# Kernel tuning notes

Hardware: AMD Instinct MI355X
Metric: run time of the kernel (lower is better)

Reference implementation:

```python
import jax, jax.numpy as jnp
import numpy as np

DT = 0.01
Ek, El, Ena = -77.0, -65.0, 55.0
Iapp, Kp, Vt, Vs = 1.5, 3.0, 20.0, 0.0
a_d, a_r = 1.0, 0.1
gk, gl, gna, gs = 35.0, 0.3, 40.0, 0.04
B, T = 100, 2000


def _safe(num, den, fallback):
    # Reproduces the torch.where singularity patch at V==25 / V==-35.
    z = den == 0
    return jnp.where(z, fallback, num / jnp.where(z, 1.0, den))


def _rates(V):
    aN = _safe(0.02 * (V - 25), 1 - jnp.exp((25 - V) / 9.0), 0.18)
    bN = _safe(-0.002 * (V - 25), 1 - jnp.exp((V - 25) / 9.0), 0.018)
    aM = _safe(0.182 * (V + 35), 1 - jnp.exp((-V - 35) / 9.0), 1.638)
    bM = _safe(-0.124 * (V + 35), 1 - jnp.exp((V + 35) / 9.0), 1.116)
    aH = 0.25 * jnp.exp((-V - 90) / 12.0)
    bH = 0.25 * jnp.exp((V + 34) / 12.0)
    return aN, bN, aM, bM, aH, bH


def _gate(a, b, prev):
    # Crank-Nicolson gate update: (a*DT + (1 - DT/2*(a+b))*prev) / (DT/2*(a+b) + 1)
    s = DT / 2 * (a + b)
    return (a * DT + (1 - s) * prev) / (s + 1)


def _hh_layer(z, y0):
    # z: (B, T, N) synaptic drive; returns full voltage history (B, T, N).
    Bn, Tn, N = z.shape
    V0 = jnp.full((Bn, N), -70.0, z.dtype)
    init = (V0, jnp.zeros_like(V0), jnp.zeros_like(V0),
            jnp.ones_like(V0), jnp.full_like(V0, y0))
    zp = jnp.transpose(z[:, :-1, :], (1, 0, 2))  # z[k-1] drives step k

    def step(c, zk):
        V, m, n, h, y = c
        p1 = gna * m ** 3 * h
        p2 = gk * n ** 4
        Gs = DT / 2 * (p1 + p2 + gl + gs * y)
        E = p1 * Ena + p2 * Ek + gl * El + gs * Vs * y
        Vn = (V * (1 - Gs) + DT * (E + Iapp)) / (1 + Gs)
        aN, bN, aM, bM, aH, bH = _rates(Vn)
        mn = _gate(aM, bM, m)
        nn = _gate(aN, bN, n)
        hn = _gate(aH, bH, h)
        yn = _gate(a_d * zk, a_r, y)
        return (Vn, mn, nn, hn, yn), Vn

    _, Vh = jax.lax.scan(step, init, zp)  # (T-1, B, N)
    return jnp.concatenate([V0[None], Vh], 0).transpose(1, 0, 2)


def setup_inputs() -> dict:
    key = jax.random.key(0)
    k1, k2, k3 = jax.random.split(key, 3)
    batch = jax.random.normal(k1, (B, T, 28 * 28), jnp.float32)
    W1 = jax.random.normal(k2, (100, 28 * 28), jnp.float32) / np.sqrt(28 * 28)
    W2 = jax.random.normal(k3, (10, 100), jnp.float32) / np.sqrt(100)
    return {"batch": batch, "W1": W1, "W2": W2}


def reference(batch, W1, W2):
    z1 = jnp.einsum('bti,oi->bto', batch, W1)          # (B,T,100)
    V1 = _hh_layer(z1, 0.0)
    T1 = jax.nn.sigmoid((V1 - Vt) / Kp)
    z2 = jnp.einsum('btn,on->bto', T1, W2)             # (B,T,10)
    V2 = _hh_layer(z2, 1.0)
    return jax.nn.sigmoid((V2 - Vt) / Kp)
```

## Files before the change

### kernel.cpp

```cpp
#include <hip/hip_runtime.h>

#define TT 2000
#define NB 100
#define N1 100
#define KIN 784
#define CT1 1998
#define NC1 10000
#define CT2 1999
#define NC2 1000
#define NPAD 112
#define KPAD 800
#define S1 128
#define NCHUNK 16

typedef __attribute__((ext_vector_type(8))) short bf16x8;
typedef __attribute__((ext_vector_type(4))) float f32x4;

__device__ __forceinline__ float rcp_f(float d) { return __builtin_amdgcn_rcpf(d); }
__device__ __forceinline__ float sigmoid3(float V) {
  return rcp_f(1.0f + __expf((20.0f - V) * (1.0f / 3.0f)));
}
__device__ __forceinline__ float sig_from_u(float u) {
  float u3 = u * u * u;
  return rcp_f(1.0f + 0.18887560f * u3);
}
__device__ __forceinline__ float gate_u(float a, float b, float p) {
  float s = 0.005f * (a + b);
  return (a * 0.01f + (1.0f - s) * p) * rcp_f(s + 1.0f);
}
__device__ __forceinline__ float hh_step(float& V, float& m, float& n, float& h,
                                         float& y, float ay, float by, float ry) {
  float p1 = 40.0f * m * m * m * h;
  float nn2 = n * n;
  float p2 = 35.0f * nn2 * nn2;
  float Gs = 0.005f * (p1 + p2 + 0.3f + 0.04f * y);
  float E = p1 * 55.0f + p2 * (-77.0f) + (0.3f * (-65.0f));
  float Vn = (V * (1.0f - Gs) + 0.01f * (E + 1.5f)) * rcp_f(1.0f + Gs);

  float u_n = __expf((25.0f - Vn) * (1.0f / 9.0f));
  float u_m = __expf((-Vn - 35.0f) * (1.0f / 9.0f));
  float aH  = 0.25f * __expf((-Vn - 90.0f) * (1.0f / 12.0f));
  float bH  = 0.25f * __expf((Vn + 34.0f) * (1.0f / 12.0f));

  float dn = 1.0f - u_n, dm = 1.0f - u_m;
  float Bn = 0.02f * (Vn - 25.0f);
  float Am = 0.182f * (Vn + 35.0f);
  if (dn == 0.0f) { Bn = 0.18f;  dn = 1.0f; }
  if (dm == 0.0f) { Am = 1.638f; dm = 1.0f; }
  float Pn = 0.005f * Bn * (1.0f + 0.1f * u_n);
  float Pm = 0.005f * Am * (1.0f + 0.6813187f * u_m);
  n = (Bn * 0.01f + (dn - Pn) * n) * rcp_f(dn + Pn);
  m = (Am * 0.01f + (dm - Pm) * m) * rcp_f(dm + Pm);
  h = gate_u(aH, bH, h);
  y = (ay + by * y) * ry;
  V = Vn;
  return u_n;
}

__device__ __forceinline__ short bf16rne(float x) {
  unsigned u = __builtin_bit_cast(unsigned, x);
  unsigned r = u + 0x7fffu + ((u >> 16) & 1u);
  return (short)(r >> 16);
}
__device__ __forceinline__ float bf2f(short s) {
  unsigned u = ((unsigned)(unsigned short)s) << 16;
  return __builtin_bit_cast(float, u);
}
__device__ __forceinline__ void bsplit(float x, short& h, short& l) {
  h = bf16rne(x);
  l = bf16rne(x - bf2f(h));
}

__global__ __launch_bounds__(256) void prep_w1(const float* __restrict__ W1,
                                               short* __restrict__ W1h,
                                               short* __restrict__ W1l) {
  int idx = blockIdx.x * 256 + threadIdx.x;
  if (idx >= NPAD * KPAD) return;
  int nrow = idx / KPAD, k = idx - nrow * KPAD;
  float v = (nrow < N1 && k < KIN) ? W1[nrow * KIN + k] : 0.0f;
  short h, l; bsplit(v, h, l);
  W1h[idx] = h; W1l[idx] = l;
}

__device__ void gemm_body(const float* __restrict__ batch, const short* __restrict__ W1h,
                          const short* __restrict__ W1l, float* __restrict__ z1s,
                          int k, int b, char* smem) {
  short (*AsH)[32] = (short(*)[32])(smem);
  short (*AsL)[32] = (short(*)[32])(smem + 8192);
  short (*BsH)[32] = (short(*)[32])(smem + 16384);
  short (*BsL)[32] = (short(*)[32])(smem + 16384 + 7168);

  const int tid = threadIdx.x;
  const int tBeg = k * S1;
  const int tEnd = (tBeg + S1 < CT1) ? (tBeg + S1) : CT1;
  const int rows = tEnd - tBeg;
  const size_t rBeg = (size_t)b * CT1 + tBeg;

  const int w = tid >> 6;
  const int lane = tid & 63;
  const int lr = lane & 15;
  const int kg = lane >> 4;
  const int srow = tid >> 1;
  const int kc = (tid & 1) * 16;
  const int brow = tid >> 1;
  const bool bAct = (tid < 224);

  int tCl = tBeg + ((srow < rows) ? srow : (rows - 1));
  const float* aSrc = batch + ((size_t)b * TT + tCl) * KIN + kc;
  const short* bhSrc = W1h + (size_t)brow * KPAD + kc;
  const short* blSrc = W1l + (size_t)brow * KPAD + kc;

  float4 a0, a1, a2, a3;
  int4 bh0, bh1, bl0, bl1;

  a0 = a1 = a2 = a3 = make_float4(0.f, 0.f, 0.f, 0.f);
  if (kc < KIN) {
    a0 = *(const float4*)(aSrc);
    a1 = *(const float4*)(aSrc + 4);
    a2 = *(const float4*)(aSrc + 8);
    a3 = *(const float4*)(aSrc + 12);
  }
  if (bAct) {
    bh0 = *(const int4*)(bhSrc);
    bh1 = *(const int4*)(bhSrc + 8);
    bl0 = *(const int4*)(blSrc);
    bl1 = *(const int4*)(blSrc + 8);
  }

  f32x4 acc[2][7];
#pragma unroll
  for (int mt = 0; mt < 2; ++mt)
#pragma unroll
    for (int nt = 0; nt < 7; ++nt) acc[mt][nt] = (f32x4){0.f, 0.f, 0.f, 0.f};

  for (int kt = 0; kt < KPAD; kt += 32) {
    __syncthreads();
    {
      float av[16] = {a0.x, a0.y, a0.z, a0.w, a1.x, a1.y, a1.z, a1.w,
                      a2.x, a2.y, a2.z, a2.w, a3.x, a3.y, a3.z, a3.w};
      bf16x8 h0, h1, l0, l1;
#pragma unroll
      for (int i = 0; i < 8; ++i) {
        short hh, ll;
        bsplit(av[i], hh, ll);     h0[i] = hh; l0[i] = ll;
        bsplit(av[8 + i], hh, ll); h1[i] = hh; l1[i] = ll;
      }
      *(bf16x8*)&AsH[srow][kc] = h0;
      *(bf16x8*)&AsH[srow][kc + 8] = h1;
      *(bf16x8*)&AsL[srow][kc] = l0;
      *(bf16x8*)&AsL[srow][kc + 8] = l1;
      if (bAct) {
        *(int4*)&BsH[brow][kc] = bh0;
        *(int4*)&BsH[brow][kc + 8] = bh1;
        *(int4*)&BsL[brow][kc] = bl0;
        *(int4*)&BsL[brow][kc + 8] = bl1;
      }
    }
    __syncthreads();

    int kn = kt + 32;
    if (kn < KPAD) {
      a0 = a1 = a2 = a3 = make_float4(0.f, 0.f, 0.f, 0.f);
      if (kn + kc < KIN) {
        a0 = *(const float4*)(aSrc + kn);
        a1 = *(const float4*)(aSrc + kn + 4);
        a2 = *(const float4*)(aSrc + kn + 8);
        a3 = *(const float4*)(aSrc + kn + 12);
      }
      if (bAct) {
        bh0 = *(const int4*)(bhSrc + kn);
        bh1 = *(const int4*)(bhSrc + kn + 8);
        bl0 = *(const int4*)(blSrc + kn);
        bl1 = *(const int4*)(blSrc + kn + 8);
      }
    }

    bf16x8 aH0 = *(bf16x8*)&AsH[w * 32 + lr][kg * 8];
    bf16x8 aH1 = *(bf16x8*)&AsH[w * 32 + 16 + lr][kg * 8];
    bf16x8 aL0 = *(bf16x8*)&AsL[w * 32 + lr][kg * 8];
    bf16x8 aL1 = *(bf16x8*)&AsL[w * 32 + 16 + lr][kg * 8];
#pragma unroll
    for (int nt = 0; nt < 7; ++nt) {
      bf16x8 bH = *(bf16x8*)&BsH[nt * 16 + lr][kg * 8];
      bf16x8 bL = *(bf16x8*)&BsL[nt * 16 + lr][kg * 8];
      acc[0][nt] = __builtin_amdgcn_mfma_f32_16x16x32_bf16(aH0, bH, acc[0][nt], 0, 0, 0);
      acc[0][nt] = __builtin_amdgcn_mfma_f32_16x16x32_bf16(aH0, bL, acc[0][nt], 0, 0, 0);
      acc[0][nt] = __builtin_amdgcn_mfma_f32_16x16x32_bf16(aL0, bH, acc[0][nt], 0, 0, 0);
      acc[1][nt] = __builtin_amdgcn_mfma_f32_16x16x32_bf16(aH1, bH, acc[1][nt], 0, 0, 0);
      acc[1][nt] = __builtin_amdgcn_mfma_f32_16x16x32_bf16(aH1, bL, acc[1][nt], 0, 0, 0);
      acc[1][nt] = __builtin_amdgcn_mfma_f32_16x16x32_bf16(aL1, bH, acc[1][nt], 0, 0, 0);
    }
  }

#pragma unroll
  for (int nt = 0; nt < 7; ++nt) {
    int n = nt * 16 + lr;
    if (n < 100) {
#pragma unroll
      for (int mt = 0; mt < 2; ++mt) {
        int rloc = w * 32 + mt * 16 + kg * 4;
        f32x4 d = acc[mt][nt];
#pragma unroll
        for (int rr = 0; rr < 4; ++rr) {
          if (rloc + rr < rows) z1s[(rBeg + rloc + rr) * 100 + n] = d[rr];
        }
      }
    }
  }
}

__device__ void l1_body(const float* __restrict__ z1s, float* __restrict__ T1s,
                        float* __restrict__ st, int k, int lb) {
  int c = lb * 256 + threadIdx.x;
  if (c >= NC1) return;
  int b = c / 100, ni = c - b * 100;
  int tBeg = k * S1;
  int tEnd = (tBeg + S1 < CT1) ? (tBeg + S1) : CT1;
  int nsteps = tEnd - tBeg;
  float* SV = st; float* SM = st + NC1; float* SN = st + 2 * NC1;
  float* SH = st + 3 * NC1; float* SY = st + 4 * NC1;
  float V, m, n, h, y;
  if (k == 0) {
    V = -70.f; m = 0.f; n = 0.f; h = 1.f; y = 0.f;
    T1s[c] = __expf((25.0f + 70.0f) * (1.0f / 9.0f));
  } else { V = SV[c]; m = SM[c]; n = SN[c]; h = SH[c]; y = SY[c]; }
  const float* zp = z1s + ((size_t)b * CT1 + tBeg) * 100 + ni;
  float* tp = T1s + (size_t)(tBeg + 1) * NC1 + c;
  float zc[8], zx[8], ay[8], by[8], ry[8];
#pragma unroll
  for (int j = 0; j < 8; ++j) zc[j] = zp[j * 100];
  zp += 800;
  int NW = nsteps >> 3, tail = nsteps & 7;
  for (int i = 0; i < NW; ++i) {
#pragma unroll
    for (int j = 0; j < 8; ++j) zx[j] = zp[j * 100];
    zp += 800;
#pragma unroll
    for (int j = 0; j < 8; ++j) {
      float s = 0.005f * zc[j] + 0.0005f;
      ay[j] = zc[j] * 0.01f; by[j] = 1.0f - s; ry[j] = rcp_f(1.0f + s);
    }
#pragma unroll
    for (int j = 0; j < 8; ++j) {
      float u = hh_step(V, m, n, h, y, ay[j], by[j], ry[j]);
      *tp = u;
      tp += NC1;
    }
#pragma unroll
    for (int j = 0; j < 8; ++j) zc[j] = zx[j];
  }
  for (int j = 0; j < tail; ++j) {
    float s = 0.005f * zc[j] + 0.0005f;
    float u = hh_step(V, m, n, h, y, zc[j] * 0.01f, 1.0f - s, rcp_f(1.0f + s));
    *tp = u;
    tp += NC1;
  }
  SV[c] = V; SM[c] = m; SN[c] = n; SH[c] = h; SY[c] = y;
}

__device__ void z2_body(const float* __restrict__ T1s, const float* __restrict__ W2,
                        float* __restrict__ z2s, int k, int zb, char* smem) {
  float* w2 = (float*)smem;
  const int tid = threadIdx.x;
  if (tid < 250) *(float4*)&w2[tid * 4] = *(const float4*)&W2[tid * 4];
  __syncthreads();
  int tBeg = k * S1;
  int tEnd = (tBeg + S1 < CT2) ? (tBeg + S1) : CT2;
  int r = tBeg * NB + zb * 256 + tid;
  if (r >= tEnd * NB) return;
  const float* in = T1s + (size_t)r * 100;
  float acc[10];
#pragma unroll
  for (int o = 0; o < 10; ++o) acc[o] = 0.f;
  for (int k4 = 0; k4 < 25; ++k4) {
    float4 v = *(const float4*)(in + k4 * 4);
    v.x = sig_from_u(v.x); v.y = sig_from_u(v.y);
    v.z = sig_from_u(v.z); v.w = sig_from_u(v.w);
#pragma unroll
    for (int o = 0; o < 10; ++o) {
      float4 w = *(const float4*)&w2[o * 100 + k4 * 4];
      acc[o] += v.x * w.x + v.y * w.y + v.z * w.z + v.w * w.w;
    }
  }
  float* op = z2s + (size_t)r * 10;
#pragma unroll
  for (int o = 0; o < 10; o += 2) *(float2*)(op + o) = make_float2(acc[o], acc[o + 1]);
}

__device__ void l2_body(const float* __restrict__ z2s, float* __restrict__ out,
                        float* __restrict__ st, int k, int lb) {
  int c2 = lb * 256 + threadIdx.x;
  if (c2 >= NC2) return;
  int b = c2 / 10, o = c2 - b * 10;
  int tBeg = k * S1;
  int tEnd = (tBeg + S1 < CT2) ? (tBeg + S1) : CT2;
  int nsteps = tEnd - tBeg;
  float* SV = st; float* SM = st + NC2; float* SN = st + 2 * NC2;
  float* SH = st + 3 * NC2; float* SY = st + 4 * NC2;
  float V, m, n, h, y;
  if (k == 0) {
    V = -70.f; m = 0.f; n = 0.f; h = 1.f; y = 1.f;
    out[(size_t)b * TT * 10 + o] = sigmoid3(-70.f);
  } else { V = SV[c2]; m = SM[c2]; n = SN[c2]; h = SH[c2]; y = SY[c2]; }
  const float* zp = z2s + (size_t)tBeg * NC2 + c2;
  float* op = out + ((size_t)b * TT + tBeg + 1) * 10 + o;
  float zc[8], zx[8], ay[8], by[8], ry[8];
#pragma unroll
  for (int j = 0; j < 8; ++j) zc[j] = zp[j * NC2];
  zp += 8 * NC2;
  int NW = nsteps >> 3, tail = nsteps & 7;
  for (int i = 0; i < NW; ++i) {
#pragma unroll
    for (int j = 0; j < 8; ++j) zx[j] = zp[j * NC2];
    zp += 8 * NC2;
#pragma unroll
    for (int j = 0; j < 8; ++j) {
      float s = 0.005f * zc[j] + 0.0005f;
      ay[j] = zc[j] * 0.01f; by[j] = 1.0f - s; ry[j] = rcp_f(1.0f + s);
    }
#pragma unroll
    for (int j = 0; j < 8; ++j) {
      float u = hh_step(V, m, n, h, y, ay[j], by[j], ry[j]);
      *op = sig_from_u(u);
      op += 10;
    }
#pragma unroll
    for (int j = 0; j < 8; ++j) zc[j] = zx[j];
  }
  for (int j = 0; j < tail; ++j) {
    float s = 0.005f * zc[j] + 0.0005f;
    float u = hh_step(V, m, n, h, y, zc[j] * 0.01f, 1.0f - s, rcp_f(1.0f + s));
    *op = sig_from_u(u);
    op += 10;
  }
  SV[c2] = V; SM[c2] = m; SN[c2] = n; SH[c2] = h; SY[c2] = y;
}

__global__ __launch_bounds__(256) void fused_pipe(
    const float* __restrict__ batch, const short* __restrict__ W1h,
    const short* __restrict__ W1l, const float* __restrict__ W2,
    float* __restrict__ z1s, float* __restrict__ T1s, float* __restrict__ z2s,
    float* __restrict__ out, float* __restrict__ stL1, float* __restrict__ stL2,
    int kG, int kL1, int kZ2, int kL2,
    int nL1, int nL2, int nZ2, int nG) {
  __shared__ __align__(16) char smem[30720];
  int bid = (int)blockIdx.x;
  if (bid < nL1) { l1_body(z1s, T1s, stL1, kL1, bid); return; }
  bid -= nL1;
  if (bid < nL2) { l2_body(z2s, out, stL2, kL2, bid); return; }
  bid -= nL2;
  if (bid < nZ2) { z2_body(T1s, W2, z2s, kZ2, bid, smem); return; }
  bid -= nZ2;
  if (bid < nG) { gemm_body(batch, W1h, W1l, z1s, kG, bid, smem); }
}

extern "C" void kernel_launch(void* const* d_in, const int* in_sizes, int n_in,
                              void* d_out, int out_size, void* d_ws, size_t ws_size,
                              hipStream_t stream) {
  (void)in_sizes; (void)n_in; (void)out_size; (void)ws_size;
  const float* batch = (const float*)d_in[0];
  const float* W1 = (const float*)d_in[1];
  const float* W2 = (const float*)d_in[2];
  float* out = (float*)d_out;

  float* z1s = (float*)d_ws;
  float* T1s = z1s + (size_t)NB * CT1 * 100 + 1600;
  float* z2s = T1s + (size_t)CT2 * NC1;
  short* W1h = (short*)(z2s + (size_t)CT2 * NC2 + 16000);
  short* W1l = W1h + (size_t)NPAD * KPAD;
  float* stL1 = (float*)(W1l + (size_t)NPAD * KPAD);
  float* stL2 = stL1 + 5 * NC1;

  prep_w1<<<dim3((NPAD * KPAD + 255) / 256), dim3(256), 0, stream>>>(W1, W1h, W1l);

  for (int d = 0; d <= NCHUNK + 2; ++d) {
    int kG = d, kL1 = d - 1, kZ2 = d - 2, kL2 = d - 3;
    int nG = (kG >= 0 && kG < NCHUNK) ? NB : 0;
    int nL1 = (kL1 >= 0 && kL1 < NCHUNK) ? (NC1 + 255) / 256 : 0;
    int nZ2 = 0;
    if (kZ2 >= 0 && kZ2 < NCHUNK) {
      int tBeg = kZ2 * S1;
      int tEnd = (tBeg + S1 < CT2) ? (tBeg + S1) : CT2;
      nZ2 = ((tEnd - tBeg) * NB + 255) / 256;
    }
    int nL2 = (kL2 >= 0 && kL2 < NCHUNK) ? (NC2 + 255) / 256 : 0;
    int grid = nL1 + nL2 + nZ2 + nG;
    if (grid == 0) continue;
    fused_pipe<<<dim3((unsigned)grid), dim3(256), 0, stream>>>(
        batch, W1h, W1l, W2, z1s, T1s, z2s, out, stL1, stL2,
        kG, kL1, kZ2, kL2, nL1, nL2, nZ2, nG);
  }
}
```

Before: 783.5 us.

## Hoist layer-1 GEMM into one upfront kernel, pipeline only scans

```diff
diff --git a/kernel.cpp b/kernel.cpp
--- a/kernel.cpp
+++ b/kernel.cpp
@@ -82,15 +82,19 @@
   W1h[idx] = h; W1l[idx] = l;
 }
 
-__device__ void gemm_body(const float* __restrict__ batch, const short* __restrict__ W1h,
-                          const short* __restrict__ W1l, float* __restrict__ z1s,
-                          int k, int b, char* smem) {
+__global__ __launch_bounds__(256) void gemm_all(const float* __restrict__ batch,
+                                                const short* __restrict__ W1h,
+                                                const short* __restrict__ W1l,
+                                                float* __restrict__ z1s) {
+  __shared__ __align__(16) char smem[30720];
   short (*AsH)[32] = (short(*)[32])(smem);
   short (*AsL)[32] = (short(*)[32])(smem + 8192);
   short (*BsH)[32] = (short(*)[32])(smem + 16384);
   short (*BsL)[32] = (short(*)[32])(smem + 16384 + 7168);
 
   const int tid = threadIdx.x;
+  const int b = (int)blockIdx.x / NCHUNK;
+  const int k = (int)blockIdx.x % NCHUNK;
   const int tBeg = k * S1;
   const int tEnd = (tBeg + S1 < CT1) ? (tBeg + S1) : CT1;
   const int rows = tEnd - tBeg;
@@ -336,22 +340,18 @@
   SV[c2] = V; SM[c2] = m; SN[c2] = n; SH[c2] = h; SY[c2] = y;
 }
 
-__global__ __launch_bounds__(256) void fused_pipe(
-    const float* __restrict__ batch, const short* __restrict__ W1h,
-    const short* __restrict__ W1l, const float* __restrict__ W2,
-    float* __restrict__ z1s, float* __restrict__ T1s, float* __restrict__ z2s,
+__global__ __launch_bounds__(256) void scan_pipe(
+    const float* __restrict__ W2,
+    const float* __restrict__ z1s, float* __restrict__ T1s, float* __restrict__ z2s,
     float* __restrict__ out, float* __restrict__ stL1, float* __restrict__ stL2,
-    int kG, int kL1, int kZ2, int kL2,
-    int nL1, int nL2, int nZ2, int nG) {
-  __shared__ __align__(16) char smem[30720];
+    int kL1, int kZ2, int kL2, int nL1, int nL2, int nZ2) {
+  __shared__ __align__(16) char smem[4096];
   int bid = (int)blockIdx.x;
   if (bid < nL1) { l1_body(z1s, T1s, stL1, kL1, bid); return; }
   bid -= nL1;
   if (bid < nL2) { l2_body(z2s, out, stL2, kL2, bid); return; }
   bid -= nL2;
-  if (bid < nZ2) { z2_body(T1s, W2, z2s, kZ2, bid, smem); return; }
-  bid -= nZ2;
-  if (bid < nG) { gemm_body(batch, W1h, W1l, z1s, kG, bid, smem); }
+  if (bid < nZ2) { z2_body(T1s, W2, z2s, kZ2, bid, smem); }
 }
 
 extern "C" void kernel_launch(void* const* d_in, const int* in_sizes, int n_in,
@@ -373,9 +373,10 @@
 
   prep_w1<<<dim3((NPAD * KPAD + 255) / 256), dim3(256), 0, stream>>>(W1, W1h, W1l);
 
-  for (int d = 0; d <= NCHUNK + 2; ++d) {
-    int kG = d, kL1 = d - 1, kZ2 = d - 2, kL2 = d - 3;
-    int nG = (kG >= 0 && kG < NCHUNK) ? NB : 0;
+  gemm_all<<<dim3(NB * NCHUNK), dim3(256), 0, stream>>>(batch, W1h, W1l, z1s);
+
+  for (int d = 0; d <= NCHUNK + 1; ++d) {
+    int kL1 = d, kZ2 = d - 1, kL2 = d - 2;
     int nL1 = (kL1 >= 0 && kL1 < NCHUNK) ? (NC1 + 255) / 256 : 0;
     int nZ2 = 0;
     if (kZ2 >= 0 && kZ2 < NCHUNK) {
@@ -384,10 +385,9 @@
       nZ2 = ((tEnd - tBeg) * NB + 255) / 256;
     }
     int nL2 = (kL2 >= 0 && kL2 < NCHUNK) ? (NC2 + 255) / 256 : 0;
-    int grid = nL1 + nL2 + nZ2 + nG;
+    int grid = nL1 + nL2 + nZ2;
     if (grid == 0) continue;
-    fused_pipe<<<dim3((unsigned)grid), dim3(256), 0, stream>>>(
-        batch, W1h, W1l, W2, z1s, T1s, z2s, out, stL1, stL2,
-        kG, kL1, kZ2, kL2, nL1, nL2, nZ2, nG);
-  }
-}
+    scan_pipe<<<dim3((unsigned)grid), dim3(256), 0, stream>>>(
+        W2, z1s, T1s, z2s, out, stL1, stL2, kL1, kZ2, kL2, nL1, nL2, nZ2);
+  }
+}
```

New measurement: 688.2 us (median of 2 runs). 12.2% less time.
